# Performance work log

Hardware: AMD Instinct MI355X
Metric: run time of the kernel (lower is better)

The kernel has to match this reference:

```python
import jax, jax.numpy as jnp
import numpy as np

DEPTH = 8
DIM = 512
D_INNER = 2 * DIM          # mamba expand=2
D_STATE = 16
D_CONV = 4
DT_RANK = DIM // 16        # 32
B, H, W = 2, 16, 16
EPS = 1e-5


def setup_inputs() -> dict:
    key = jax.random.key(0)
    ks = jax.random.split(key, 8)
    s = 0.02
    f32 = jnp.float32
    x = jax.random.normal(ks[0], (B, DIM, H, W), f32)
    in_proj_w = (jax.random.normal(ks[1], (DEPTH, 2 * D_INNER, DIM), f32) * s)
    conv_w = (jax.random.normal(ks[2], (DEPTH, D_INNER, D_CONV), f32) * 0.1)
    conv_b = jnp.zeros((DEPTH, D_INNER), f32)
    x_proj_w = (jax.random.normal(ks[3], (DEPTH, DT_RANK + 2 * D_STATE, D_INNER), f32) * s)
    dt_proj_w = (jax.random.normal(ks[4], (DEPTH, D_INNER, DT_RANK), f32) * s)
    dt_proj_b = (jax.random.normal(ks[5], (DEPTH, D_INNER), f32) * 0.1)
    # S4D-real init: A = -exp(A_log), A_log = log(1..d_state)
    A_log = jnp.log(jnp.broadcast_to(
        jnp.arange(1, D_STATE + 1, dtype=f32), (DEPTH, D_INNER, D_STATE)))
    D = jnp.ones((DEPTH, D_INNER), f32)
    out_proj_w = (jax.random.normal(ks[6], (DEPTH, DIM, D_INNER), f32) * s)
    norm_w = jnp.ones((DEPTH, DIM), f32)
    final_norm_w = jnp.ones((DIM,), f32)
    return {"x": x, "in_proj_w": in_proj_w, "conv_w": conv_w, "conv_b": conv_b,
            "x_proj_w": x_proj_w, "dt_proj_w": dt_proj_w, "dt_proj_b": dt_proj_b,
            "A_log": A_log, "D": D, "out_proj_w": out_proj_w,
            "norm_w": norm_w, "final_norm_w": final_norm_w}


def _rmsnorm(x, w):
    # rms_norm_ref: no mean subtraction, weight only (bias is None)
    return x * jax.lax.rsqrt(jnp.mean(x * x, axis=-1, keepdims=True) + EPS) * w


def _mixer(h, Wi, cw, cb, Wx, Wdt, bdt, A_log, Dv, Wo):
    # h: [B, L, DIM]
    xz = jnp.einsum('bld,ed->ble', h, Wi)            # [B,L,2*Di]
    xc, z = jnp.split(xz, 2, axis=-1)
    # causal depthwise conv1d (pad left d_conv-1), then SiLU
    xt = xc.transpose(0, 2, 1)                        # [B,Di,L]
    xt = jax.lax.conv_general_dilated(
        xt, cw[:, None, :], (1,), [(D_CONV - 1, 0)],
        feature_group_count=D_INNER)
    xc = jax.nn.silu((xt + cb[None, :, None]).transpose(0, 2, 1))  # [B,L,Di]
    dbl = jnp.einsum('bld,kd->blk', xc, Wx)           # [B,L,dt_rank+2N]
    dtr = dbl[..., :DT_RANK]
    Bm = dbl[..., DT_RANK:DT_RANK + D_STATE]          # [B,L,N]
    Cm = dbl[..., DT_RANK + D_STATE:]                 # [B,L,N]
    dt = jax.nn.softplus(jnp.einsum('blr,dr->bld', dtr, Wdt) + bdt)  # [B,L,Di]
    A = -jnp.exp(A_log)                               # [Di,N]
    dA = jnp.exp(dt[..., None] * A)                   # [B,L,Di,N]
    dBx = (dt * xc)[..., None] * Bm[:, :, None, :]    # [B,L,Di,N]

    def step(s, inp):
        a, bx, c = inp
        s = a * s + bx                                # [B,Di,N]
        return s, jnp.einsum('bdn,bn->bd', s, c)

    s0 = jnp.zeros((xc.shape[0], D_INNER, D_STATE), xc.dtype)
    _, ys = jax.lax.scan(step, s0, (dA.transpose(1, 0, 2, 3),
                                    dBx.transpose(1, 0, 2, 3),
                                    Cm.transpose(1, 0, 2)))
    y = ys.transpose(1, 0, 2) + Dv * xc               # [B,L,Di]
    y = y * jax.nn.silu(z)
    return jnp.einsum('bld,od->blo', y, Wo)           # [B,L,DIM]


def reference(x, in_proj_w, conv_w, conv_b, x_proj_w, dt_proj_w, dt_proj_b,
              A_log, D, out_proj_w, norm_w, final_norm_w):
    Bz, C, Hh, Ww = x.shape
    h = x.reshape(Bz, C, Hh * Ww).transpose(0, 2, 1)  # [B,L,C]
    residual = None
    for i in range(DEPTH):
        # fused add + RMSNorm (prenorm): residual <- h + residual; hn = norm(residual)
        residual = h if residual is None else h + residual
        hn = _rmsnorm(residual, norm_w[i])
        h = _mixer(hn, in_proj_w[i], conv_w[i], conv_b[i], x_proj_w[i],
                   dt_proj_w[i], dt_proj_b[i], A_log[i], D[i], out_proj_w[i])
    # Original module: with return_index=[depth-1], the returned tensor is the
    # post-loop `residual`; the final mixer output and final norm are dead code.
    out = residual.reshape(Bz, Hh, Ww, C)
    return out.transpose(0, 3, 1, 2)
```

## Files before the change

### kernel.cpp

```cpp
#include <hip/hip_runtime.h>
#include <hip/hip_bf16.h>

typedef __bf16 bf16x8 __attribute__((ext_vector_type(8)));
typedef float  f32x4  __attribute__((ext_vector_type(4)));
typedef unsigned short ushort8v __attribute__((ext_vector_type(8)));

#define DIM    512
#define DINNER 1024
#define SEQL   256
#define NLAYER 7
#define LPAD   260
#define NCH    8
#define CLEN   32

#define N4WI (NLAYER * 2048 * 512 / 4)
#define N4WX (NLAYER * 64 * 1024 / 4)
#define N4WO (NLAYER * 512 * 1024 / 4)
#define N4ALL (N4WI + N4WX + N4WO)
#define NCASTB (N4ALL / 256)

__global__ __launch_bounds__(256) void k_castin(const float* __restrict__ Wi,
                                                const float* __restrict__ Wx,
                                                const float* __restrict__ Wo,
                                                const float* __restrict__ x,
                                                __hip_bfloat16* __restrict__ wib,
                                                __hip_bfloat16* __restrict__ wxb,
                                                __hip_bfloat16* __restrict__ wob,
                                                float* __restrict__ res) {
  if (blockIdx.x >= NCASTB) {
    int idx = (blockIdx.x - NCASTB) * 256 + threadIdx.x;
    int d = idx & (DIM - 1), l = (idx >> 9) & (SEQL - 1), b = idx >> 17;
    res[idx] = x[((size_t)((b << 9) + d) << 8) + l];
    return;
  }
  int i = blockIdx.x * 256 + threadIdx.x;
  const float* src; __hip_bfloat16* dst; int j;
  if (i < N4WI)             { src = Wi; dst = wib; j = i; }
  else if (i < N4WI + N4WX) { src = Wx; dst = wxb; j = i - N4WI; }
  else                      { src = Wo; dst = wob; j = i - N4WI - N4WX; }
  float4 v = reinterpret_cast<const float4*>(src)[j];
  struct alignas(8) B4 { __hip_bfloat16 a, b, c, d; };
  B4 o{ (__hip_bfloat16)v.x, (__hip_bfloat16)v.y, (__hip_bfloat16)v.z, (__hip_bfloat16)v.w };
  reinterpret_cast<B4*>(dst)[j] = o;
}

__global__ __launch_bounds__(1024) void k_front(const float* __restrict__ res,
                                                const float* __restrict__ nwL,
                                                const __hip_bfloat16* __restrict__ wiL,
                                                const float4* __restrict__ cwL,
                                                const float* __restrict__ cbL,
                                                __hip_bfloat16* __restrict__ xcb,
                                                float* __restrict__ xcT,
                                                float* __restrict__ zT) {
  __shared__ __align__(16) char smem[75264];
  __hip_bfloat16 (*s_hn)[520] = (__hip_bfloat16(*)[520])smem;
  float (*s_xz)[132] = (float(*)[132])(smem + 49920);
  float (*s_sv)[68]  = (float(*)[68])smem;
  const int tid = threadIdx.x, bid = blockIdx.x;
  const int wid = tid >> 6, lane = tid & 63;
  const int r = lane & 15, g = lane >> 4;
  const int ttile = bid >> 4, sl = bid & 15;
  const int t0 = ttile * 32, m0 = t0 - 3;
#pragma unroll
  for (int k = 0; k < 3; ++k) {
    int rw = wid * 3 + k;
    int grc = min(max(m0 + rw, 0), 511);
    const float* rr = res + ((size_t)grc << 9);
    float v[8]; float ssum = 0.f;
#pragma unroll
    for (int j2 = 0; j2 < 8; ++j2) { v[j2] = rr[lane + (j2 << 6)]; ssum = fmaf(v[j2], v[j2], ssum); }
#pragma unroll
    for (int m = 1; m < 64; m <<= 1) ssum += __shfl_xor(ssum, m);
    float inv = rsqrtf(ssum * (1.0f / 512.0f) + 1e-5f);
#pragma unroll
    for (int j2 = 0; j2 < 8; ++j2)
      s_hn[rw][lane + (j2 << 6)] = (__hip_bfloat16)(v[j2] * inv * nwL[lane + (j2 << 6)]);
  }
  __syncthreads();
  for (int j = wid; j < 24; j += 16) {
    int mf = j >> 3, cf = j & 7;
    int gcol = (cf < 4) ? (sl * 64 + cf * 16 + r) : (1024 + sl * 64 + (cf - 4) * 16 + r);
    const bf16x8* pb = reinterpret_cast<const bf16x8*>(wiL + (size_t)gcol * 512) + g;
    f32x4 acc = {0.f, 0.f, 0.f, 0.f};
#pragma unroll
    for (int kc = 0; kc < 16; ++kc) {
      bf16x8 a = *reinterpret_cast<const bf16x8*>(&s_hn[mf * 16 + r][kc * 32 + g * 8]);
      acc = __builtin_amdgcn_mfma_f32_16x16x32_bf16(a, pb[kc * 4], acc, 0, 0, 0);
    }
    int cc = (cf < 4) ? (cf * 16 + r) : (64 + (cf - 4) * 16 + r);
#pragma unroll
    for (int jj = 0; jj < 4; ++jj) s_xz[mf * 16 + g * 4 + jj][cc] = acc[jj];
  }
  __syncthreads();
  const int t0s = t0 & 255;
#pragma unroll
  for (int k = 0; k < 2; ++k) {
    int e = tid + (k << 10);
    int lloc = e >> 6, c = e & 63;
    int gd = sl * 64 + c;
    int lseq = t0s + lloc;
    float4 wv = cwL[gd];
    float accv = cbL[gd];
    accv = fmaf(s_xz[lloc + 3][c], wv.w, accv);
    if (lseq >= 1) accv = fmaf(s_xz[lloc + 2][c], wv.z, accv);
    if (lseq >= 2) accv = fmaf(s_xz[lloc + 1][c], wv.y, accv);
    if (lseq >= 3) accv = fmaf(s_xz[lloc + 0][c], wv.x, accv);
    float sv = accv / (1.f + __expf(-accv));
    xcb[(size_t)(t0 + lloc) * 1024 + gd] = (__hip_bfloat16)sv;
    s_sv[lloc][c] = sv;
  }
  __syncthreads();
#pragma unroll
  for (int k = 0; k < 2; ++k) {
    int e = tid + (k << 10);
    int lloc = e & 31, c = e >> 5;
    int gd = sl * 64 + c;
    int token = t0 + lloc;
    xcT[(size_t)gd * 512 + token] = s_sv[lloc][c];
    zT [(size_t)gd * 512 + token] = s_xz[lloc + 3][64 + c];
  }
}

__global__ __launch_bounds__(1024) void k_xdt(const __hip_bfloat16* __restrict__ xcb,
                                              const __hip_bfloat16* __restrict__ wxL,
                                              float* __restrict__ dblBC,
                                              __hip_bfloat16* __restrict__ dtrb) {
  __shared__ __align__(16) float s_red[4 * 1088];
  const int tid = threadIdx.x, bid = blockIdx.x;
  const int wid = tid >> 6, lane = tid & 63;
  const int r = lane & 15, g = lane >> 4;
  const int t0 = bid * 16;
  {
    int nf = wid >> 2, ks = wid & 3;
    const bf16x8* pa = reinterpret_cast<const bf16x8*>(xcb + (size_t)(t0 + r) * 1024) + ks * 32 + g;
    const bf16x8* pb = reinterpret_cast<const bf16x8*>(wxL + (size_t)(nf * 16 + r) * 1024) + ks * 32 + g;
    f32x4 acc = {0.f, 0.f, 0.f, 0.f};
#pragma unroll
    for (int kc = 0; kc < 8; ++kc)
      acc = __builtin_amdgcn_mfma_f32_16x16x32_bf16(pa[kc * 4], pb[kc * 4], acc, 0, 0, 0);
#pragma unroll
    for (int jj = 0; jj < 4; ++jj)
      s_red[ks * 1088 + (g * 4 + jj) * 68 + nf * 16 + r] = acc[jj];
  }
  __syncthreads();
  {
    int row = tid >> 6, col = tid & 63;
    float dsum = s_red[row * 68 + col] + s_red[1088 + row * 68 + col]
               + s_red[2176 + row * 68 + col] + s_red[3264 + row * 68 + col];
    if (col >= 32) dblBC[((size_t)(t0 + row) << 5) + (col - 32)] = dsum;
    else           dtrb [((size_t)(t0 + row) << 5) + col] = (__hip_bfloat16)dsum;
  }
}

__global__ __launch_bounds__(1024) void k_scan(const float* __restrict__ dblBC,
                                               const __hip_bfloat16* __restrict__ dtrb,
                                               const float* __restrict__ WdtL,
                                               const float* __restrict__ bdtL,
                                               const float* __restrict__ xcT,
                                               const float* __restrict__ zT,
                                               const float* __restrict__ alog,
                                               const float* __restrict__ dv,
                                               __hip_bfloat16* __restrict__ y) {
  __shared__ __align__(16) char smem[127744];
  float (*s_dt)[LPAD] = (float(*)[LPAD])(smem);
  float (*s_xc)[LPAD] = (float(*)[LPAD])(smem + 8320);
  float (*s_B)[LPAD]  = (float(*)[LPAD])(smem + 16640);
  float (*s_C)[LPAD]  = (float(*)[LPAD])(smem + 33280);
  float (*s_cp)[68]   = (float(*)[68]) (smem + 49920);
  float (*s_pe)[128]  = (float(*)[128])(smem + 119552);
  float (*s_se)[128]  = (float(*)[128])(smem + 123648);
  const int tid = threadIdx.x, bid = blockIdx.x;
  const int cg = tid >> 7;
  const int tt = tid & 127;
  const int n = tt & 15, dl = tt >> 4;
  const int b = bid >> 7;
  const int d0 = (bid & 127) << 3;
  const int d = d0 + dl;
  const int bL = b * SEQL;

#pragma unroll
  for (int k = 0; k < 2; ++k) {
    int fidx = tid + (k << 10);
    int l = fidx >> 3, q = fidx & 7;
    float4 v = *reinterpret_cast<const float4*>(dblBC + ((size_t)(bL + l) << 5) + (q << 2));
    float* dst = (q < 4) ? &s_B[(q & 3) << 2][l] : &s_C[(q & 3) << 2][l];
    dst[0] = v.x; dst[LPAD] = v.y; dst[2 * LPAD] = v.z; dst[3 * LPAD] = v.w;
  }
  if (tid < 512) {
    int dd = tid >> 6, c4 = tid & 63;
    float4 v = *reinterpret_cast<const float4*>(xcT + (size_t)(d0 + dd) * 512 + bL + (c4 << 2));
    *reinterpret_cast<float4*>(&s_xc[dd][c4 << 2]) = v;
  }
  {
    int tk = tid >> 2;
    int cp = (tid & 3) << 1;
    const ushort8v* drp = reinterpret_cast<const ushort8v*>(
        reinterpret_cast<const unsigned short*>(dtrb) + ((size_t)(bL + tk) << 5));
    float xv[32];
#pragma unroll
    for (int q = 0; q < 4; ++q) {
      ushort8v u = drp[q];
#pragma unroll
      for (int e = 0; e < 8; ++e)
        xv[q * 8 + e] = __uint_as_float(((unsigned int)u[e]) << 16);
    }
#pragma unroll
    for (int kk = 0; kk < 2; ++kk) {
      int ch = cp + kk;
      const float4* wr = reinterpret_cast<const float4*>(WdtL + ((size_t)(d0 + ch) << 5));
      float acc = bdtL[d0 + ch];
#pragma unroll
      for (int q = 0; q < 8; ++q) {
        float4 w = wr[q];
        acc = fmaf(xv[q * 4 + 0], w.x, acc);
        acc = fmaf(xv[q * 4 + 1], w.y, acc);
        acc = fmaf(xv[q * 4 + 2], w.z, acc);
        acc = fmaf(xv[q * 4 + 3], w.w, acc);
      }
      s_dt[ch][tk] = (acc > 20.f) ? acc : log1pf(__expf(acc));
    }
  }
  __syncthreads();

  const float An = -__expf(alog[(size_t)d * 16 + n]);
  const int lb = cg << 5;

  float s = 0.f, P = 1.f;
#pragma unroll 2
  for (int l4 = 0; l4 < CLEN; l4 += 4) {
    const int l = lb + l4;
    float4 dt4 = *reinterpret_cast<const float4*>(&s_dt[dl][l]);
    float4 xc4 = *reinterpret_cast<const float4*>(&s_xc[dl][l]);
    float4 B4  = *reinterpret_cast<const float4*>(&s_B[n][l]);
    float dA;
    dA = __expf(dt4.x * An); P *= dA; s = fmaf(dA, s, dt4.x * xc4.x * B4.x);
    dA = __expf(dt4.y * An); P *= dA; s = fmaf(dA, s, dt4.y * xc4.y * B4.y);
    dA = __expf(dt4.z * An); P *= dA; s = fmaf(dA, s, dt4.z * xc4.z * B4.z);
    dA = __expf(dt4.w * An); P *= dA; s = fmaf(dA, s, dt4.w * xc4.w * B4.w);
  }
  s_pe[cg][tt] = P;
  s_se[cg][tt] = s;
  __syncthreads();

  float ss = 0.f;
  for (int c = 0; c < cg; ++c) ss = fmaf(s_pe[c][tt], ss, s_se[c][tt]);

  float s2 = ss;
#pragma unroll 2
  for (int l4 = 0; l4 < CLEN; l4 += 4) {
    const int l = lb + l4;
    float4 dt4 = *reinterpret_cast<const float4*>(&s_dt[dl][l]);
    float4 xc4 = *reinterpret_cast<const float4*>(&s_xc[dl][l]);
    float4 B4  = *reinterpret_cast<const float4*>(&s_B[n][l]);
    float4 C4  = *reinterpret_cast<const float4*>(&s_C[n][l]);
    float dA, c;
    dA = __expf(dt4.x * An); s2 = fmaf(dA, s2, dt4.x * xc4.x * B4.x); c = s2 * C4.x;
    c += __shfl_xor(c, 1); if (!(n & 1)) s_cp[l + 0][(dl << 3) | (n >> 1)] = c;
    dA = __expf(dt4.y * An); s2 = fmaf(dA, s2, dt4.y * xc4.y * B4.y); c = s2 * C4.y;
    c += __shfl_xor(c, 1); if (!(n & 1)) s_cp[l + 1][(dl << 3) | (n >> 1)] = c;
    dA = __expf(dt4.z * An); s2 = fmaf(dA, s2, dt4.z * xc4.z * B4.z); c = s2 * C4.z;
    c += __shfl_xor(c, 1); if (!(n & 1)) s_cp[l + 2][(dl << 3) | (n >> 1)] = c;
    dA = __expf(dt4.w * An); s2 = fmaf(dA, s2, dt4.w * xc4.w * B4.w); c = s2 * C4.w;
    c += __shfl_xor(c, 1); if (!(n & 1)) s_cp[l + 3][(dl << 3) | (n >> 1)] = c;
  }
  __syncthreads();

#pragma unroll
  for (int k = 0; k < 2; ++k) {
    int idx = tid + (k << 10);
    int l = idx >> 3, dd = idx & 7;
    const float* cr = &s_cp[l][dd << 3];
    float4 a0 = *reinterpret_cast<const float4*>(cr);
    float4 a1 = *reinterpret_cast<const float4*>(cr + 4);
    float sum = ((a0.x + a0.y) + (a0.z + a0.w)) + ((a1.x + a1.y) + (a1.z + a1.w));
    float xcv = s_xc[dd][l];
    float zv = zT[(size_t)(d0 + dd) * 512 + bL + l];
    float yv = (sum + dv[d0 + dd] * xcv) * (zv / (1.f + __expf(-zv)));
    y[((size_t)(bL + l) << 10) + d0 + dd] = (__hip_bfloat16)yv;
  }
}

template <bool FINAL>
__global__ __launch_bounds__(1024) void k_outproj(const __hip_bfloat16* __restrict__ y,
                                                  const __hip_bfloat16* __restrict__ woL,
                                                  float* __restrict__ res,
                                                  float* __restrict__ out) {
  __shared__ __align__(16) float s_red[16 * 1088 + 32 * 33];
  float (*s_tr)[33] = (float(*)[33])(s_red + 16 * 1088);
  const int tid = threadIdx.x, bid = blockIdx.x;
  const int wid = tid >> 6, lane = tid & 63;
  const int r = lane & 15, g = lane >> 4;
  int tile = bid >> 2, q = bid & 3;
  int row0 = (tile >> 3) * 64 + ((q >> 1) << 5);
  int col0 = (tile & 7) * 64 + ((q & 1) << 5);
  {
    const bf16x8* pa0 = reinterpret_cast<const bf16x8*>(y + (size_t)(row0 + r) * 1024) + g + wid * 8;
    const bf16x8* pa1 = reinterpret_cast<const bf16x8*>(y + (size_t)(row0 + 16 + r) * 1024) + g + wid * 8;
    const bf16x8* pb0 = reinterpret_cast<const bf16x8*>(woL + (size_t)(col0 + r) * 1024) + g + wid * 8;
    const bf16x8* pb1 = reinterpret_cast<const bf16x8*>(woL + (size_t)(col0 + 16 + r) * 1024) + g + wid * 8;
    f32x4 zz = {0.f, 0.f, 0.f, 0.f};
    f32x4 acc[4] = {zz, zz, zz, zz};
#pragma unroll
    for (int kc = 0; kc < 2; ++kc) {
      bf16x8 a0 = pa0[kc * 4], a1 = pa1[kc * 4];
      bf16x8 b0 = pb0[kc * 4], b1 = pb1[kc * 4];
      acc[0] = __builtin_amdgcn_mfma_f32_16x16x32_bf16(a0, b0, acc[0], 0, 0, 0);
      acc[1] = __builtin_amdgcn_mfma_f32_16x16x32_bf16(a0, b1, acc[1], 0, 0, 0);
      acc[2] = __builtin_amdgcn_mfma_f32_16x16x32_bf16(a1, b0, acc[2], 0, 0, 0);
      acc[3] = __builtin_amdgcn_mfma_f32_16x16x32_bf16(a1, b1, acc[3], 0, 0, 0);
    }
    float* sr = s_red + wid * 1088;
#pragma unroll
    for (int e = 0; e < 4; ++e)
#pragma unroll
      for (int jj = 0; jj < 4; ++jj)
        sr[(((e >> 1) << 4) + (g << 2) + jj) * 34 + ((e & 1) << 4) + r] = acc[e][jj];
  }
  __syncthreads();
  {
    int rrow = tid >> 5, rcol = tid & 31;
    float sum = 0.f;
#pragma unroll
    for (int w = 0; w < 16; ++w) sum += s_red[w * 1088 + rrow * 34 + rcol];
    if (!FINAL) {
      res[(size_t)(row0 + rrow) * 512 + col0 + rcol] += sum;
    } else {
      s_tr[rcol][rrow] = res[(size_t)(row0 + rrow) * 512 + col0 + rcol] + sum;
    }
  }
  if (FINAL) {
    __syncthreads();
    int tl = tid & 31, tc = tid >> 5;
    int b = row0 >> 8, l0 = row0 & 255;
    out[(((size_t)((b << 9) + col0 + tc)) << 8) | (l0 + tl)] = s_tr[tc][tl];
  }
}

extern "C" void kernel_launch(void* const* d_in, const int* in_sizes, int n_in,
                              void* d_out, int out_size, void* d_ws, size_t ws_size,
                              hipStream_t stream) {
  (void)in_sizes; (void)n_in; (void)out_size; (void)ws_size;
  const float* x    = (const float*)d_in[0];
  const float* Wi   = (const float*)d_in[1];
  const float* cw   = (const float*)d_in[2];
  const float* cb   = (const float*)d_in[3];
  const float* Wx   = (const float*)d_in[4];
  const float* Wdt  = (const float*)d_in[5];
  const float* bdt  = (const float*)d_in[6];
  const float* Alog = (const float*)d_in[7];
  const float* Dv   = (const float*)d_in[8];
  const float* Wo   = (const float*)d_in[9];
  const float* nw   = (const float*)d_in[10];

  char* ws = (char*)d_ws;
  float*          res   = (float*)(ws + 0);
  __hip_bfloat16* xcb   = (__hip_bfloat16*)(ws + 1048576);
  float*          xcT   = (float*)(ws + 2097152);
  float*          zT    = (float*)(ws + 4194304);
  __hip_bfloat16* dtrb  = (__hip_bfloat16*)(ws + 6291456);
  float*          dblBC = (float*)(ws + 8388608);
  __hip_bfloat16* y     = (__hip_bfloat16*)(ws + 8454144);
  __hip_bfloat16* wib   = (__hip_bfloat16*)(ws + 10485760);
  __hip_bfloat16* wxb   = (__hip_bfloat16*)(ws + 25165824);
  __hip_bfloat16* wob   = (__hip_bfloat16*)(ws + 26083328);

  k_castin<<<NCASTB + 1024, 256, 0, stream>>>(Wi, Wx, Wo, x, wib, wxb, wob, res);

  for (int L = 0; L < NLAYER; ++L) {
    k_front<<<256, 1024, 0, stream>>>(res, nw + L * DIM,
                                      wib + (size_t)L * 2048 * 512,
                                      (const float4*)cw + (size_t)L * DINNER,
                                      cb + L * DINNER, xcb, xcT, zT);
    k_xdt<<<32, 1024, 0, stream>>>(xcb, wxb + (size_t)L * 64 * 1024, dblBC, dtrb);
    k_scan<<<256, 1024, 0, stream>>>(dblBC, dtrb,
                                     Wdt + (size_t)L * DINNER * 32, bdt + L * DINNER,
                                     xcT, zT,
                                     Alog + (size_t)L * DINNER * 16, Dv + L * DINNER, y);
    if (L < NLAYER - 1)
      k_outproj<false><<<256, 1024, 0, stream>>>(y, wob + (size_t)L * 512 * 1024, res, nullptr);
    else
      k_outproj<true><<<256, 1024, 0, stream>>>(y, wob + (size_t)L * 512 * 1024, res, (float*)d_out);
  }
}
```

Measured before the change: 352.1 us.

## Fuse x_proj GEMM into scan kernel, recomputing per block

Removes the separate k_xdt launch and folds the x_proj GEMM (256 tokens x 64 outputs x 1024) into each k_scan block. Every block recomputes the full per-batch dbl matrix with MFMA, staging Wx tiles in shared memory that aliases the B/C buffers, then transposes B and C into their smem layout and reads dt_rank values from shared memory in fp32. This drops one launch per layer plus the global round trip for dblBC and dtrb. In exchange it adds redundant GEMM work, since 128 blocks per batch each recompute the same product, and it adds extra syncs inside each scan block.

```diff
diff --git a/kernel.cpp b/kernel.cpp
--- a/kernel.cpp
+++ b/kernel.cpp
@@ -3,7 +3,6 @@
 
 typedef __bf16 bf16x8 __attribute__((ext_vector_type(8)));
 typedef float  f32x4  __attribute__((ext_vector_type(4)));
-typedef unsigned short ushort8v __attribute__((ext_vector_type(8)));
 
 #define DIM    512
 #define DINNER 1024
@@ -121,39 +120,8 @@
   }
 }
 
-__global__ __launch_bounds__(1024) void k_xdt(const __hip_bfloat16* __restrict__ xcb,
-                                              const __hip_bfloat16* __restrict__ wxL,
-                                              float* __restrict__ dblBC,
-                                              __hip_bfloat16* __restrict__ dtrb) {
-  __shared__ __align__(16) float s_red[4 * 1088];
-  const int tid = threadIdx.x, bid = blockIdx.x;
-  const int wid = tid >> 6, lane = tid & 63;
-  const int r = lane & 15, g = lane >> 4;
-  const int t0 = bid * 16;
-  {
-    int nf = wid >> 2, ks = wid & 3;
-    const bf16x8* pa = reinterpret_cast<const bf16x8*>(xcb + (size_t)(t0 + r) * 1024) + ks * 32 + g;
-    const bf16x8* pb = reinterpret_cast<const bf16x8*>(wxL + (size_t)(nf * 16 + r) * 1024) + ks * 32 + g;
-    f32x4 acc = {0.f, 0.f, 0.f, 0.f};
-#pragma unroll
-    for (int kc = 0; kc < 8; ++kc)
-      acc = __builtin_amdgcn_mfma_f32_16x16x32_bf16(pa[kc * 4], pb[kc * 4], acc, 0, 0, 0);
-#pragma unroll
-    for (int jj = 0; jj < 4; ++jj)
-      s_red[ks * 1088 + (g * 4 + jj) * 68 + nf * 16 + r] = acc[jj];
-  }
-  __syncthreads();
-  {
-    int row = tid >> 6, col = tid & 63;
-    float dsum = s_red[row * 68 + col] + s_red[1088 + row * 68 + col]
-               + s_red[2176 + row * 68 + col] + s_red[3264 + row * 68 + col];
-    if (col >= 32) dblBC[((size_t)(t0 + row) << 5) + (col - 32)] = dsum;
-    else           dtrb [((size_t)(t0 + row) << 5) + col] = (__hip_bfloat16)dsum;
-  }
-}
-
-__global__ __launch_bounds__(1024) void k_scan(const float* __restrict__ dblBC,
-                                               const __hip_bfloat16* __restrict__ dtrb,
+__global__ __launch_bounds__(1024) void k_scan(const __hip_bfloat16* __restrict__ xcb,
+                                               const __hip_bfloat16* __restrict__ wxL,
                                                const float* __restrict__ WdtL,
                                                const float* __restrict__ bdtL,
                                                const float* __restrict__ xcT,
@@ -169,40 +137,71 @@
   float (*s_cp)[68]   = (float(*)[68]) (smem + 49920);
   float (*s_pe)[128]  = (float(*)[128])(smem + 119552);
   float (*s_se)[128]  = (float(*)[128])(smem + 123648);
+  __hip_bfloat16 (*s_wx)[136] = (__hip_bfloat16(*)[136])(smem + 16640);
   const int tid = threadIdx.x, bid = blockIdx.x;
+  const int wid = tid >> 6, lane = tid & 63;
   const int cg = tid >> 7;
   const int tt = tid & 127;
   const int n = tt & 15, dl = tt >> 4;
+  const int r = lane & 15, g = lane >> 4;
   const int b = bid >> 7;
   const int d0 = (bid & 127) << 3;
   const int d = d0 + dl;
   const int bL = b * SEQL;
 
-#pragma unroll
-  for (int k = 0; k < 2; ++k) {
-    int fidx = tid + (k << 10);
-    int l = fidx >> 3, q = fidx & 7;
-    float4 v = *reinterpret_cast<const float4*>(dblBC + ((size_t)(bL + l) << 5) + (q << 2));
-    float* dst = (q < 4) ? &s_B[(q & 3) << 2][l] : &s_C[(q & 3) << 2][l];
-    dst[0] = v.x; dst[LPAD] = v.y; dst[2 * LPAD] = v.z; dst[3 * LPAD] = v.w;
-  }
   if (tid < 512) {
     int dd = tid >> 6, c4 = tid & 63;
     float4 v = *reinterpret_cast<const float4*>(xcT + (size_t)(d0 + dd) * 512 + bL + (c4 << 2));
     *reinterpret_cast<float4*>(&s_xc[dd][c4 << 2]) = v;
   }
+
   {
-    int tk = tid >> 2;
-    int cp = (tid & 3) << 1;
-    const ushort8v* drp = reinterpret_cast<const ushort8v*>(
-        reinterpret_cast<const unsigned short*>(dtrb) + ((size_t)(bL + tk) << 5));
+    f32x4 zz = {0.f, 0.f, 0.f, 0.f};
+    f32x4 ga[4] = {zz, zz, zz, zz};
+    const size_t arow = (size_t)(bL + (wid << 4) + r) * 1024;
+    for (int kt = 0; kt < 8; ++kt) {
+      {
+        int row = tid >> 4, cc = tid & 15;
+        *reinterpret_cast<bf16x8*>(&s_wx[row][cc << 3]) =
+            *reinterpret_cast<const bf16x8*>(wxL + (size_t)row * 1024 + (kt << 7) + (cc << 3));
+      }
+      __syncthreads();
+      const bf16x8* pa = reinterpret_cast<const bf16x8*>(xcb + arow + (kt << 7)) + g;
+#pragma unroll
+      for (int kc = 0; kc < 4; ++kc) {
+        bf16x8 a = pa[kc * 4];
+#pragma unroll
+        for (int nf = 0; nf < 4; ++nf) {
+          bf16x8 bf = *reinterpret_cast<const bf16x8*>(&s_wx[(nf << 4) + r][(kc << 5) + (g << 3)]);
+          ga[nf] = __builtin_amdgcn_mfma_f32_16x16x32_bf16(a, bf, ga[nf], 0, 0, 0);
+        }
+      }
+      __syncthreads();
+    }
+#pragma unroll
+    for (int nf = 0; nf < 4; ++nf)
+#pragma unroll
+      for (int jj = 0; jj < 4; ++jj)
+        s_cp[(wid << 4) + (g << 2) + jj][(nf << 4) + r] = ga[nf][jj];
+  }
+  __syncthreads();
+
+#pragma unroll
+  for (int k = 0; k < 4; ++k) {
+    int idx = tid + (k << 10);
+    int l = idx >> 4, nn = idx & 15;
+    s_B[nn][l] = s_cp[l][32 + nn];
+    s_C[nn][l] = s_cp[l][48 + nn];
+  }
+  {
+    int tk = tid >> 2, cp = (tid & 3) << 1;
     float xv[32];
-#pragma unroll
-    for (int q = 0; q < 4; ++q) {
-      ushort8v u = drp[q];
-#pragma unroll
-      for (int e = 0; e < 8; ++e)
-        xv[q * 8 + e] = __uint_as_float(((unsigned int)u[e]) << 16);
+    const float* drow = &s_cp[tk][0];
+#pragma unroll
+    for (int q = 0; q < 8; ++q) {
+      float4 x4 = *reinterpret_cast<const float4*>(drow + (q << 2));
+      xv[q * 4 + 0] = x4.x; xv[q * 4 + 1] = x4.y;
+      xv[q * 4 + 2] = x4.z; xv[q * 4 + 3] = x4.w;
     }
 #pragma unroll
     for (int kk = 0; kk < 2; ++kk) {
@@ -357,8 +356,6 @@
   __hip_bfloat16* xcb   = (__hip_bfloat16*)(ws + 1048576);
   float*          xcT   = (float*)(ws + 2097152);
   float*          zT    = (float*)(ws + 4194304);
-  __hip_bfloat16* dtrb  = (__hip_bfloat16*)(ws + 6291456);
-  float*          dblBC = (float*)(ws + 8388608);
   __hip_bfloat16* y     = (__hip_bfloat16*)(ws + 8454144);
   __hip_bfloat16* wib   = (__hip_bfloat16*)(ws + 10485760);
   __hip_bfloat16* wxb   = (__hip_bfloat16*)(ws + 25165824);
@@ -371,8 +368,7 @@
                                       wib + (size_t)L * 2048 * 512,
                                       (const float4*)cw + (size_t)L * DINNER,
                                       cb + L * DINNER, xcb, xcT, zT);
-    k_xdt<<<32, 1024, 0, stream>>>(xcb, wxb + (size_t)L * 64 * 1024, dblBC, dtrb);
-    k_scan<<<256, 1024, 0, stream>>>(dblBC, dtrb,
+    k_scan<<<256, 1024, 0, stream>>>(xcb, wxb + (size_t)L * 64 * 1024,
                                      Wdt + (size_t)L * DINNER * 32, bdt + L * DINNER,
                                      xcT, zT,
                                      Alog + (size_t)L * DINNER * 16, Dv + L * DINNER, y);
```

After: 426.6 us. 21.1% more time.
